# Kernel tuning notes

Measured on AMD Instinct MI355X. Metric: run time of the kernel, lower is better.

The kernel has to match this reference:

```python
import jax, jax.numpy as jnp
import numpy as np

BS, DIM, HID, T = 4096, 64, 256, 101
GAMMA = 0.1
EPS = 1e-12  # pinverse guard for the 1x1 matrix G G^T


def setup_inputs() -> dict:
    key = jax.random.key(0)
    k0, k1, k2, k3 = jax.random.split(key, 4)
    return {
        "y0": jax.random.normal(k0, (BS, DIM), dtype=jnp.float32),
        "t": jnp.linspace(0.0, 1.0, T).astype(jnp.float32),
        "W1": jax.random.normal(k1, (DIM, HID), dtype=jnp.float32) * 0.05,
        "b1": jnp.zeros((HID,), dtype=jnp.float32),
        "W2": jax.random.normal(k2, (HID, DIM), dtype=jnp.float32) * 0.05,
        "b2": jnp.zeros((DIM,), dtype=jnp.float32),
        "wg": jax.random.normal(k3, (DIM,), dtype=jnp.float32) * 0.1,
        "bg": jnp.zeros((), dtype=jnp.float32),
    }


def reference(y0, t, W1, b1, W2, b2, wg, bg):
    # f_model: 2-layer tanh MLP (ignores t, as is common for autonomous dynamics)
    def f_model(ti, u):
        return jnp.tanh(u @ W1 + b1) @ W2 + b2  # (bs, dim)

    # g_fn: scalar constraint per sample
    def g_single(ui):
        return jnp.tanh(ui @ wg + bg)  # scalar

    def dynamic(ti, u):
        f_u = f_model(ti, u)                              # (bs, dim)
        g_u = jax.vmap(g_single)(u)                       # (bs,)
        # Torch detaches u before autograd Jacobian (create_graph keeps param path)
        G = jax.vmap(jax.grad(g_single))(jax.lax.stop_gradient(u))  # (bs, dim) == G_u row
        # F_u = G^T (G G^T)^+ ; G G^T is 1x1 -> scalar pinverse
        s = jnp.sum(G * G, axis=-1)                       # (bs,)
        pinv = jnp.where(jnp.abs(s) > EPS, 1.0 / s, 0.0)  # (bs,)
        stable = GAMMA * (g_u * pinv)[:, None] * G        # (bs, dim)
        return f_u - stable

    dt = t[1] - t[0]  # Euler solver uses constant dt

    def step(y, ti):
        y_new = y + dynamic(ti, y) * dt
        return y_new, y_new

    _, ys = jax.lax.scan(step, y0, t[:-1])
    return jnp.concatenate([y0[None], ys], axis=0)  # (T, bs, dim)
```

## Files before the change

kernel.cpp:

```cpp
#include <hip/hip_runtime.h>
#include <hip/hip_bf16.h>


#define GAMMA 0.1f
#define EPSG  1e-12f

typedef __attribute__((ext_vector_type(8))) short bf16x8;
typedef __attribute__((ext_vector_type(4))) float f32x4;

__device__ __forceinline__ float ftanh(float x) {
    float e = __expf(2.0f * x);
    return 1.0f - 2.0f * __builtin_amdgcn_rcpf(e + 1.0f);
}

__device__ __forceinline__ unsigned int f2bf(float f) {
    unsigned int u = __float_as_uint(f);
    return (u + 0x7fffu + ((u >> 16) & 1u)) >> 16;
}

__device__ __forceinline__ unsigned int pack2(float lo, float hi) {
    union { __hip_bfloat162 h; unsigned int u; } cv;
    cv.h = __float22bfloat162_rn(float2{lo, hi});
    return cv.u;
}

#define BARRIER_LGKM() asm volatile("s_waitcnt lgkmcnt(0)\ns_barrier" ::: "memory")

__device__ __forceinline__ int kperm(int lg, int j) {
    return lg * 4 + (j >> 1) + ((j & 1) << 4);
}

__global__ __launch_bounds__(512, 1) void snde_kernel(
    const float* __restrict__ y0, const float* __restrict__ t,
    const float* __restrict__ W1, const float* __restrict__ b1,
    const float* __restrict__ W2, const float* __restrict__ b2,
    const float* __restrict__ wg, const float* __restrict__ bgp,
    float* __restrict__ out)
{
    __shared__ unsigned short uAs[16 * 64];
    __shared__ unsigned int   hp[16 * 128];
    __shared__ __align__(16) float zs[16];

    const int tid = threadIdx.x;
    const int w   = tid >> 6;
    const int l   = tid & 63;
    const int l15 = l & 15;
    const int lg  = l >> 4;
    const int nt  = w & 3;
    const int s0g = blockIdx.x * 16;

    bf16x8 B1[2][2];
    #pragma unroll
    for (int ntt = 0; ntt < 2; ++ntt) {
        const int n = w * 32 + ntt * 16 + l15;
        #pragma unroll
        for (int kt = 0; kt < 2; ++kt) {
            bf16x8 v;
            #pragma unroll
            for (int j = 0; j < 8; ++j)
                v[j] = (short)f2bf(W1[(kt * 32 + lg * 8 + j) * 256 + n]);
            B1[ntt][kt] = v;
        }
    }
    bf16x8 B2[8];
    #pragma unroll
    for (int kt = 0; kt < 8; ++kt) {
        const int n = nt * 16 + l15;
        bf16x8 v;
        #pragma unroll
        for (int j = 0; j < 8; ++j)
            v[j] = (short)f2bf(W2[(kt * 32 + kperm(lg, j)) * 64 + n]);
        B2[kt] = v;
    }
    bf16x8 Bz[2];
    #pragma unroll
    for (int kt = 0; kt < 2; ++kt) {
        bf16x8 v;
        #pragma unroll
        for (int j = 0; j < 8; ++j)
            v[j] = (l15 == 0) ? (short)f2bf(wg[kt * 32 + lg * 8 + j]) : (short)0;
        Bz[kt] = v;
    }

    float b1v[2];
    #pragma unroll
    for (int ntt = 0; ntt < 2; ++ntt) b1v[ntt] = b1[w * 32 + ntt * 16 + l15];
    const float b2v = b2[nt * 16 + l15];
    const float wgv = wg[nt * 16 + l15];
    float wsum = wg[l] * wg[l];
    #pragma unroll
    for (int m = 1; m < 64; m <<= 1) wsum += __shfl_xor(wsum, m, 64);
    const float bg  = bgp[0];
    const float dtv = t[1] - t[0];

    float uold[4];
    if (w < 4) {
        #pragma unroll
        for (int i = 0; i < 4; ++i) {
            const int s = lg * 4 + i;
            const int c = nt * 16 + l15;
            uold[i] = y0[(size_t)(s0g + s) * 64 + c];
            unsigned int boff = ((unsigned)(s * 128 + c * 2)) ^ (((unsigned)(s & 7)) << 4);
            *(unsigned short*)((char*)uAs + boff) = (unsigned short)f2bf(uold[i]);
            out[(size_t)(s0g + s) * 64 + c] = uold[i];
        }
    }
    __syncthreads();

    for (int step = 0; step < 100; ++step) {
        bf16x8 A1[2];
        #pragma unroll
        for (int kt = 0; kt < 2; ++kt) {
            unsigned int boff = ((unsigned)(l15 * 128 + (kt * 32 + lg * 8) * 2))
                              ^ (((unsigned)(l15 & 7)) << 4);
            A1[kt] = *(const bf16x8*)((const char*)uAs + boff);
        }
        f32x4 acc1[2];
        #pragma unroll
        for (int ntt = 0; ntt < 2; ++ntt) {
            acc1[ntt][0] = b1v[ntt]; acc1[ntt][1] = b1v[ntt];
            acc1[ntt][2] = b1v[ntt]; acc1[ntt][3] = b1v[ntt];
        }
        #pragma unroll
        for (int ntt = 0; ntt < 2; ++ntt)
            #pragma unroll
            for (int kt = 0; kt < 2; ++kt)
                acc1[ntt] = __builtin_amdgcn_mfma_f32_16x16x32_bf16(A1[kt], B1[ntt][kt], acc1[ntt], 0, 0, 0);

        if (w == 4) {
            f32x4 accz = {0.f, 0.f, 0.f, 0.f};
            #pragma unroll
            for (int kt = 0; kt < 2; ++kt)
                accz = __builtin_amdgcn_mfma_f32_16x16x32_bf16(A1[kt], Bz[kt], accz, 0, 0, 0);
            if (l15 == 0) *(f32x4*)(&zs[lg * 4]) = accz;
        }

        #pragma unroll
        for (int i = 0; i < 4; ++i) {
            const int m = lg * 4 + i;
            const unsigned int pk = pack2(ftanh(acc1[0][i]), ftanh(acc1[1][i]));
            unsigned int boff = ((unsigned)(m * 512 + (w * 16 + l15) * 4))
                              ^ (((unsigned)(m & 7)) << 4);
            *(unsigned int*)((char*)hp + boff) = pk;
        }
        BARRIER_LGKM();

        if (w < 4) {
            const f32x4 z4 = *(const f32x4*)(&zs[lg * 4]);
            bf16x8 A2[8];
            #pragma unroll
            for (int kt = 0; kt < 8; ++kt) {
                unsigned int boff = ((unsigned)(l15 * 512 + (kt * 16 + lg * 4) * 4))
                                  ^ (((unsigned)(l15 & 7)) << 4);
                A2[kt] = *(const bf16x8*)((const char*)hp + boff);
            }
            f32x4 cf;
            #pragma unroll
            for (int i = 0; i < 4; ++i) {
                const float th = ftanh(z4[i] + bg);
                const float qq = 1.0f - th * th;
                const float sg = qq * qq * wsum;
                const float pinv = (fabsf(sg) > EPSG) ? __builtin_amdgcn_rcpf(sg) : 0.0f;
                cf[i] = GAMMA * th * pinv * qq;
            }
            f32x4 accA, accB, accC, accD;
            accA[0] = b2v; accA[1] = b2v; accA[2] = b2v; accA[3] = b2v;
            accB[0] = 0.f; accB[1] = 0.f; accB[2] = 0.f; accB[3] = 0.f;
            accC = accB; accD = accB;
            accA = __builtin_amdgcn_mfma_f32_16x16x32_bf16(A2[0], B2[0], accA, 0, 0, 0);
            accB = __builtin_amdgcn_mfma_f32_16x16x32_bf16(A2[1], B2[1], accB, 0, 0, 0);
            accC = __builtin_amdgcn_mfma_f32_16x16x32_bf16(A2[2], B2[2], accC, 0, 0, 0);
            accD = __builtin_amdgcn_mfma_f32_16x16x32_bf16(A2[3], B2[3], accD, 0, 0, 0);
            accA = __builtin_amdgcn_mfma_f32_16x16x32_bf16(A2[4], B2[4], accA, 0, 0, 0);
            accB = __builtin_amdgcn_mfma_f32_16x16x32_bf16(A2[5], B2[5], accB, 0, 0, 0);
            accC = __builtin_amdgcn_mfma_f32_16x16x32_bf16(A2[6], B2[6], accC, 0, 0, 0);
            accD = __builtin_amdgcn_mfma_f32_16x16x32_bf16(A2[7], B2[7], accD, 0, 0, 0);

            const int c = nt * 16 + l15;
            float* orow = &out[(size_t)(step + 1) * (4096 * 64) + (size_t)(s0g + lg * 4) * 64 + c];
            #pragma unroll
            for (int i = 0; i < 4; ++i) {
                const float f  = (accA[i] + accB[i]) + (accC[i] + accD[i]);
                const float un = uold[i] + (f - cf[i] * wgv) * dtv;
                uold[i] = un;
                const int s = lg * 4 + i;
                unsigned int boff = ((unsigned)(s * 128 + c * 2)) ^ (((unsigned)(s & 7)) << 4);
                *(unsigned short*)((char*)uAs + boff) = (unsigned short)f2bf(un);
                orow[i * 64] = un;
            }
        }
        BARRIER_LGKM();
    }
}

extern "C" void kernel_launch(void* const* d_in, const int* in_sizes, int n_in,
                              void* d_out, int out_size, void* d_ws, size_t ws_size,
                              hipStream_t stream) {
    const float* y0 = (const float*)d_in[0];
    const float* t  = (const float*)d_in[1];
    const float* W1 = (const float*)d_in[2];
    const float* b1 = (const float*)d_in[3];
    const float* W2 = (const float*)d_in[4];
    const float* b2 = (const float*)d_in[5];
    const float* wg = (const float*)d_in[6];
    const float* bg = (const float*)d_in[7];
    float* out = (float*)d_out;

    snde_kernel<<<dim3(256), dim3(512), 0, stream>>>(y0, t, W1, b1, W2, b2, wg, bg, out);
}
```

Before: 93.36 us.

## Split second-layer K reduction across all eight waves with LDS partial sums

The second matmul (hidden to output) previously ran on only four of eight waves, each doing eight MFMAs. Now all eight waves each do four MFMAs over half of the K dimension. The upper waves write partial sums to a new shared buffer, and the lower waves add them in after an extra barrier. This halves the serial MFMA chain on the critical path, at the cost of one more block-wide barrier per step plus extra LDS traffic.

```diff
diff --git a/kernel.cpp b/kernel.cpp
--- a/kernel.cpp
+++ b/kernel.cpp
@@ -40,6 +40,7 @@
     __shared__ unsigned short uAs[16 * 64];
     __shared__ unsigned int   hp[16 * 128];
     __shared__ __align__(16) float zs[16];
+    __shared__ __align__(16) float fx[4][64][4];
 
     const int tid = threadIdx.x;
     const int w   = tid >> 6;
@@ -47,6 +48,7 @@
     const int l15 = l & 15;
     const int lg  = l >> 4;
     const int nt  = w & 3;
+    const int kh  = w >> 2;
     const int s0g = blockIdx.x * 16;
 
     bf16x8 B1[2][2];
@@ -62,15 +64,16 @@
             B1[ntt][kt] = v;
         }
     }
-    bf16x8 B2[8];
-    #pragma unroll
-    for (int kt = 0; kt < 8; ++kt) {
-        const int n = nt * 16 + l15;
+    bf16x8 B2[4];
+    #pragma unroll
+    for (int kj = 0; kj < 4; ++kj) {
+        const int kt = kh * 4 + kj;
+        const int n  = nt * 16 + l15;
         bf16x8 v;
         #pragma unroll
         for (int j = 0; j < 8; ++j)
             v[j] = (short)f2bf(W2[(kt * 32 + kperm(lg, j)) * 64 + n]);
-        B2[kt] = v;
+        B2[kj] = v;
     }
     bf16x8 Bz[2];
     #pragma unroll
@@ -145,16 +148,27 @@
         }
         BARRIER_LGKM();
 
+        f32x4 z4;
+        if (w < 4) z4 = *(const f32x4*)(&zs[lg * 4]);
+        bf16x8 A2[4];
+        #pragma unroll
+        for (int kj = 0; kj < 4; ++kj) {
+            const int kt = kh * 4 + kj;
+            unsigned int boff = ((unsigned)(l15 * 512 + (kt * 16 + lg * 4) * 4))
+                              ^ (((unsigned)(l15 & 7)) << 4);
+            A2[kj] = *(const bf16x8*)((const char*)hp + boff);
+        }
+        f32x4 accA, accB;
+        const float seed = (w < 4) ? b2v : 0.f;
+        accA[0] = seed; accA[1] = seed; accA[2] = seed; accA[3] = seed;
+        accB[0] = 0.f;  accB[1] = 0.f;  accB[2] = 0.f;  accB[3] = 0.f;
+        accA = __builtin_amdgcn_mfma_f32_16x16x32_bf16(A2[0], B2[0], accA, 0, 0, 0);
+        accB = __builtin_amdgcn_mfma_f32_16x16x32_bf16(A2[1], B2[1], accB, 0, 0, 0);
+        accA = __builtin_amdgcn_mfma_f32_16x16x32_bf16(A2[2], B2[2], accA, 0, 0, 0);
+        accB = __builtin_amdgcn_mfma_f32_16x16x32_bf16(A2[3], B2[3], accB, 0, 0, 0);
+
+        f32x4 cf;
         if (w < 4) {
-            const f32x4 z4 = *(const f32x4*)(&zs[lg * 4]);
-            bf16x8 A2[8];
-            #pragma unroll
-            for (int kt = 0; kt < 8; ++kt) {
-                unsigned int boff = ((unsigned)(l15 * 512 + (kt * 16 + lg * 4) * 4))
-                                  ^ (((unsigned)(l15 & 7)) << 4);
-                A2[kt] = *(const bf16x8*)((const char*)hp + boff);
-            }
-            f32x4 cf;
             #pragma unroll
             for (int i = 0; i < 4; ++i) {
                 const float th = ftanh(z4[i] + bg);
@@ -163,24 +177,21 @@
                 const float pinv = (fabsf(sg) > EPSG) ? __builtin_amdgcn_rcpf(sg) : 0.0f;
                 cf[i] = GAMMA * th * pinv * qq;
             }
-            f32x4 accA, accB, accC, accD;
-            accA[0] = b2v; accA[1] = b2v; accA[2] = b2v; accA[3] = b2v;
-            accB[0] = 0.f; accB[1] = 0.f; accB[2] = 0.f; accB[3] = 0.f;
-            accC = accB; accD = accB;
-            accA = __builtin_amdgcn_mfma_f32_16x16x32_bf16(A2[0], B2[0], accA, 0, 0, 0);
-            accB = __builtin_amdgcn_mfma_f32_16x16x32_bf16(A2[1], B2[1], accB, 0, 0, 0);
-            accC = __builtin_amdgcn_mfma_f32_16x16x32_bf16(A2[2], B2[2], accC, 0, 0, 0);
-            accD = __builtin_amdgcn_mfma_f32_16x16x32_bf16(A2[3], B2[3], accD, 0, 0, 0);
-            accA = __builtin_amdgcn_mfma_f32_16x16x32_bf16(A2[4], B2[4], accA, 0, 0, 0);
-            accB = __builtin_amdgcn_mfma_f32_16x16x32_bf16(A2[5], B2[5], accB, 0, 0, 0);
-            accC = __builtin_amdgcn_mfma_f32_16x16x32_bf16(A2[6], B2[6], accC, 0, 0, 0);
-            accD = __builtin_amdgcn_mfma_f32_16x16x32_bf16(A2[7], B2[7], accD, 0, 0, 0);
-
+        } else {
+            f32x4 ps;
+            ps[0] = accA[0] + accB[0]; ps[1] = accA[1] + accB[1];
+            ps[2] = accA[2] + accB[2]; ps[3] = accA[3] + accB[3];
+            *(f32x4*)(&fx[nt][l][0]) = ps;
+        }
+        BARRIER_LGKM();
+
+        if (w < 4) {
+            const f32x4 pp = *(const f32x4*)(&fx[nt][l][0]);
             const int c = nt * 16 + l15;
             float* orow = &out[(size_t)(step + 1) * (4096 * 64) + (size_t)(s0g + lg * 4) * 64 + c];
             #pragma unroll
             for (int i = 0; i < 4; ++i) {
-                const float f  = (accA[i] + accB[i]) + (accC[i] + accD[i]);
+                const float f  = (accA[i] + accB[i]) + pp[i];
                 const float un = uold[i] + (f - cf[i] * wgv) * dtv;
                 uold[i] = un;
                 const int s = lg * 4 + i;
```

Result: slower. 96.98 us (+3.9%).
